# Performance work log

Hardware: AMD Instinct MI355X
Metric: run time of the kernel (lower is better)

Reference implementation:

```python
import jax, jax.numpy as jnp
import numpy as np

D_MODEL = 1024
N_HEADS = 16
HEAD_DIM = D_MODEL // N_HEADS


def setup_inputs() -> dict:
    key = jax.random.key(0)
    kx, kq, kk, kv, ko = jax.random.split(key, 5)
    B, T = 4, 2048
    s = 1.0 / np.sqrt(D_MODEL)
    return {
        "x": jax.random.normal(kx, (B, T, D_MODEL), dtype=jnp.float32),
        "W_Q": jax.random.normal(kq, (D_MODEL, D_MODEL), dtype=jnp.float32) * s,
        "W_K": jax.random.normal(kk, (D_MODEL, D_MODEL), dtype=jnp.float32) * s,
        "W_V": jax.random.normal(kv, (D_MODEL, D_MODEL), dtype=jnp.float32) * s,
        "W_O": jax.random.normal(ko, (D_MODEL, D_MODEL), dtype=jnp.float32) * s,
    }


def reference(x, W_Q, W_K, W_V, W_O):
    B, T, C = x.shape
    H, hd = N_HEADS, HEAD_DIM
    # nn.Linear applies x @ W.T; W_* here are the [out,in] weight matrices.
    def proj(W):
        return (x @ W.T).reshape(B, T, H, hd).transpose(0, 2, 1, 3)  # [B,H,T,hd]
    q, k, v = proj(W_Q), proj(W_K), proj(W_V)
    scale = 1.0 / np.sqrt(hd).astype(np.float32)
    attn = jnp.einsum("bhqd,bhkd->bhqk", q, k) * scale  # [B,H,T,T]
    causal = jnp.tril(jnp.ones((T, T), dtype=bool))
    attn = jnp.where(causal, attn, -jnp.inf)
    attn = jax.nn.softmax(attn, axis=-1)
    out = jnp.einsum("bhqk,bhkd->bhqd", attn, v)  # [B,H,T,hd]
    out = out.transpose(0, 2, 1, 3).reshape(B, T, C)
    return out @ W_O.T
```

## Files before the change

### kernel.cpp

```cpp
#include <hip/hip_runtime.h>
#include <hip/hip_bf16.h>
#include <stdint.h>


typedef __attribute__((ext_vector_type(8))) short short8;
typedef __attribute__((ext_vector_type(4))) short short4v;
typedef __attribute__((ext_vector_type(4))) float floatx4;

#define LOG2E 1.4426950408889634f

__device__ __forceinline__ void gload_lds16(const void* g, void* l) {
  __builtin_amdgcn_global_load_lds(
      (const __attribute__((address_space(1))) void*)g,
      (__attribute__((address_space(3))) void*)l, 16, 0, 0);
}

__device__ __forceinline__ short f2bf(float f) {
  __hip_bfloat16 h = __float2bfloat16(f);
  return *reinterpret_cast<short*>(&h);
}

__global__ __launch_bounds__(256) void cvt_f32_bf16(const float* __restrict__ src,
                                                    short* __restrict__ dst, int n4,
                                                    float scale) {
  const int i = blockIdx.x * blockDim.x + threadIdx.x;
  if (i >= n4) return;
  const float4 v = reinterpret_cast<const float4*>(src)[i];
  short4v o;
  o.x = f2bf(v.x * scale); o.y = f2bf(v.y * scale);
  o.z = f2bf(v.z * scale); o.w = f2bf(v.w * scale);
  reinterpret_cast<short4v*>(dst)[i] = o;
}

__global__ __launch_bounds__(256) void cvt_weights(const float* __restrict__ wq,
                                                   const float* __restrict__ wk,
                                                   const float* __restrict__ wv,
                                                   const float* __restrict__ wo,
                                                   short* __restrict__ dst0,
                                                   float qscale) {
  const int y = blockIdx.y;
  const float* src = (y == 0) ? wq : (y == 1) ? wk : (y == 2) ? wv : wo;
  const float scale = (y == 0) ? qscale : 1.0f;
  short* dst = dst0 + (size_t)y * 1048576;
  const int i = blockIdx.x * blockDim.x + threadIdx.x;
  const float4 v = reinterpret_cast<const float4*>(src)[i];
  short4v o;
  o.x = f2bf(v.x * scale); o.y = f2bf(v.y * scale);
  o.z = f2bf(v.z * scale); o.w = f2bf(v.w * scale);
  reinterpret_cast<short4v*>(&dst[i * 4])[0] = o;
}

__global__ __launch_bounds__(512) void gemm_qkv(
    const short* __restrict__ xb, const short* __restrict__ wqkv,
    short* __restrict__ Qb, short* __restrict__ Kb, short* __restrict__ Vt) {
  __shared__ short lds_a[3][256 * 32];
  __shared__ short lds_b[3][3 * 128 * 32];
  const int tid = threadIdx.x;
  const int lane = tid & 63;
  const int w = tid >> 6;
  const int wm = w >> 1, wn = w & 1;
  const int lrow = lane & 15, lgrp = lane >> 4;

  const int flat = blockIdx.x;
  const int n0 = (flat & 7) * 128;
  const int m0 = (flat >> 3) * 256;

  floatx4 acc[3][4][4] = {};

  const int srow = tid >> 2;
  const int scb = (tid & 3) ^ (srow & 3) ^ ((srow & 4) >> 1);
  const short* ag = xb + (size_t)(m0 + srow) * 1024 + scb * 8;
  const short* bg = wqkv + (size_t)(n0 + srow) * 1024 + scb * 8;

  auto stage5 = [&](short* la, short* lb) {
    gload_lds16(ag, la + tid * 8);
    gload_lds16(ag + 128 * 1024, la + (512 + tid) * 8);
    gload_lds16(bg,           lb + tid * 8);
    gload_lds16(bg + 1048576, lb + 4096 + tid * 8);
    gload_lds16(bg + 2097152, lb + 8192 + tid * 8);
    ag += 32; bg += 32;
  };

  const int slA = (lgrp ^ (lrow & 3) ^ ((lrow & 4) >> 1)) * 8;

  auto tile = [&](const short* la, const short* lb, short* na, short* nb, bool pf) {
    if (pf) stage5(na, nb);
    short8 af[4];
#pragma unroll
    for (int mf = 0; mf < 4; ++mf)
      af[mf] = *reinterpret_cast<const short8*>(
          &la[(wm * 64 + mf * 16 + lrow) * 32 + slA]);
#pragma unroll
    for (int z = 0; z < 3; ++z) {
      short8 bf[4];
#pragma unroll
      for (int nf = 0; nf < 4; ++nf)
        bf[nf] = *reinterpret_cast<const short8*>(
            &lb[z * 4096 + (wn * 64 + nf * 16 + lrow) * 32 + slA]);
      __builtin_amdgcn_s_setprio(1);
#pragma unroll
      for (int mf = 0; mf < 4; ++mf)
#pragma unroll
        for (int nf = 0; nf < 4; ++nf)
          acc[z][mf][nf] = __builtin_amdgcn_mfma_f32_16x16x32_bf16(
              af[mf], bf[nf], acc[z][mf][nf], 0, 0, 0);
      __builtin_amdgcn_s_setprio(0);
    }
  };

  auto tiletop = [&](int n) {
    __builtin_amdgcn_sched_barrier(0);
    if (n == 0)
      asm volatile("s_waitcnt vmcnt(0)" ::: "memory");
    else
      asm volatile("s_waitcnt vmcnt(5)" ::: "memory");
    __builtin_amdgcn_s_barrier();
    __builtin_amdgcn_sched_barrier(0);
  };

  stage5(lds_a[0], lds_b[0]);
  stage5(lds_a[1], lds_b[1]);

#pragma unroll 1
  for (int kt = 0; kt < 30; kt += 3) {
    tiletop(5); tile(lds_a[0], lds_b[0], lds_a[2], lds_b[2], true);
    tiletop(5); tile(lds_a[1], lds_b[1], lds_a[0], lds_b[0], true);
    tiletop(5); tile(lds_a[2], lds_b[2], lds_a[1], lds_b[1], true);
  }
  tiletop(5); tile(lds_a[0], lds_b[0], nullptr, nullptr, false);
  tiletop(0); tile(lds_a[1], lds_b[1], nullptr, nullptr, false);

#pragma unroll
  for (int z = 0; z < 3; ++z) {
#pragma unroll
    for (int mf = 0; mf < 4; ++mf) {
#pragma unroll
      for (int nf = 0; nf < 4; ++nf) {
        if (z == 2) {
          short4v pk;
#pragma unroll
          for (int r = 0; r < 4; ++r) pk[r] = f2bf(acc[z][mf][nf][r]);
          const int t0 = m0 + wm * 64 + mf * 16 + lgrp * 4;
          const int ch = n0 + wn * 64 + nf * 16 + lrow;
          const int bh = ((t0 >> 11) << 4) + (ch >> 6);
          *reinterpret_cast<short4v*>(
              &Vt[(size_t)bh * 131072 + (size_t)(ch & 63) * 2048 + (t0 & 2047)]) = pk;
        } else {
          short* C = (z == 0) ? Qb : Kb;
#pragma unroll
          for (int r = 0; r < 4; ++r) {
            const int grow = m0 + wm * 64 + mf * 16 + lgrp * 4 + r;
            const int gcol = n0 + wn * 64 + nf * 16 + lrow;
            C[(size_t)grow * 1024 + gcol] = f2bf(acc[z][mf][nf][r]);
          }
        }
      }
    }
  }
}

template <int MODE>
__device__ __forceinline__ void gemm256_body(const short* __restrict__ A,
                                             const short* __restrict__ B,
                                             void* __restrict__ Cout,
                                             int m0, int n0,
                                             short* __restrict__ la0,
                                             short* __restrict__ la1,
                                             short* __restrict__ la2,
                                             short* __restrict__ lb0,
                                             short* __restrict__ lb1,
                                             short* __restrict__ lb2) {
  const int tid = threadIdx.x;
  const int lane = tid & 63;
  const int w = tid >> 6;
  const int wm = w >> 1, wn = w & 1;
  const int lrow = lane & 15, lgrp = lane >> 4;

  floatx4 acc[4][4] = {};

  const int srow = tid >> 2;
  const int scb = (tid & 3) ^ (srow & 3) ^ ((srow & 4) >> 1);
  const short* ag = A + (size_t)(m0 + srow) * 1024 + scb * 8;
  const short* bg = B + (size_t)(n0 + srow) * 1024 + scb * 8;

  auto stage3 = [&](short* la, short* lb) {
    gload_lds16(ag, la + tid * 8);
    gload_lds16(ag + 128 * 1024, la + (512 + tid) * 8);
    gload_lds16(bg, lb + tid * 8);
    ag += 32; bg += 32;
  };

  const int slA = (lgrp ^ (lrow & 3) ^ ((lrow & 4) >> 1)) * 8;

  auto tile = [&](const short* la, const short* lb, short* na, short* nb, bool pf) {
    if (pf) stage3(na, nb);
    short8 af[4], bf[4];
#pragma unroll
    for (int mf = 0; mf < 4; ++mf) {
      const int row = wm * 64 + mf * 16 + lrow;
      af[mf] = *reinterpret_cast<const short8*>(&la[row * 32 + slA]);
    }
#pragma unroll
    for (int nf = 0; nf < 4; ++nf) {
      const int row = wn * 64 + nf * 16 + lrow;
      bf[nf] = *reinterpret_cast<const short8*>(&lb[row * 32 + slA]);
    }
    __builtin_amdgcn_s_setprio(1);
#pragma unroll
    for (int mf = 0; mf < 4; ++mf)
#pragma unroll
      for (int nf = 0; nf < 4; ++nf)
        acc[mf][nf] = __builtin_amdgcn_mfma_f32_16x16x32_bf16(af[mf], bf[nf], acc[mf][nf], 0, 0, 0);
    __builtin_amdgcn_s_setprio(0);
  };

  auto tiletop = [&](int n) {
    __builtin_amdgcn_sched_barrier(0);
    if (n == 0)
      asm volatile("s_waitcnt vmcnt(0)" ::: "memory");
    else
      asm volatile("s_waitcnt vmcnt(3)" ::: "memory");
    __builtin_amdgcn_s_barrier();
    __builtin_amdgcn_sched_barrier(0);
  };

  stage3(la0, lb0);
  stage3(la1, lb1);

#pragma unroll 1
  for (int kt = 0; kt < 30; kt += 3) {
    tiletop(3); tile(la0, lb0, la2, lb2, true);
    tiletop(3); tile(la1, lb1, la0, lb0, true);
    tiletop(3); tile(la2, lb2, la1, lb1, true);
  }
  tiletop(3); tile(la0, lb0, nullptr, nullptr, false);
  tiletop(0); tile(la1, lb1, nullptr, nullptr, false);

#pragma unroll
  for (int mf = 0; mf < 4; ++mf) {
#pragma unroll
    for (int nf = 0; nf < 4; ++nf) {
#pragma unroll
      for (int r = 0; r < 4; ++r) {
        const int grow = m0 + wm * 64 + mf * 16 + lgrp * 4 + r;
        const int gcol = n0 + wn * 64 + nf * 16 + lrow;
        if (MODE == 1)
          reinterpret_cast<short*>(Cout)[(size_t)grow * 1024 + gcol] = f2bf(acc[mf][nf][r]);
        else
          reinterpret_cast<float*>(Cout)[(size_t)grow * 1024 + gcol] = acc[mf][nf][r];
      }
    }
  }
}

__global__ __launch_bounds__(512) void gemm_out(const short* __restrict__ Ob,
                                                const short* __restrict__ wo,
                                                float* __restrict__ out) {
  __shared__ short lds_a[3][256 * 32];
  __shared__ short lds_b[3][128 * 32];
  const int flat = blockIdx.x;
  const int xcd = flat & 7, rest = flat >> 3;
  const int nblk = rest & 7, pg = rest >> 3;
  const int panel = pg * 8 + xcd;
  gemm256_body<0>(Ob, wo, out, panel * 256, nblk * 128,
                  lds_a[0], lds_a[1], lds_a[2], lds_b[0], lds_b[1], lds_b[2]);
}

__global__ __launch_bounds__(256, 4) void attn_fwd(const short* __restrict__ Q,
                                                   const short* __restrict__ K,
                                                   const short* __restrict__ Vt,
                                                   short* __restrict__ O) {
  __shared__ short lds_k[2][64 * 64];
  __shared__ short lds_v[2][64 * 64];
  __shared__ short lds_p[4][16 * 64];

  const int tid = threadIdx.x;
  const int lane = tid & 63;
  const int w = tid >> 6;
  const int lrow = lane & 15, lgrp = lane >> 4;
  const int flat = blockIdx.x;
  const int bh = flat & 63;
  const int p = flat >> 6;
  const int qc = 4 * (((p & 3) + (p >> 2)) & 3) + (p >> 2);
  const int b = bh >> 4, h = bh & 15;

  const size_t base = (size_t)b * 2048 * 1024 + h * 64;
  const size_t vbase = (size_t)bh * 131072;

  const int srow = tid >> 3;
  const int scb = (tid & 7) ^ (srow & 7);
  const size_t koff = (size_t)srow * 1024 + scb * 8;
  const size_t voff = (size_t)srow * 2048 + scb * 8;
  short* const kd0 = &lds_k[0][tid * 8];
  short* const kd1 = &lds_k[1][tid * 8];
  short* const vd0 = &lds_v[0][tid * 8];
  short* const vd1 = &lds_v[1][tid * 8];

  auto stageK = [&](short* ldst, const short* gsrc) {
    gload_lds16(gsrc, ldst);
    gload_lds16(gsrc + 32 * 1024, ldst + 2048);
  };
  auto stageV = [&](short* ldst, const short* gsrc) {
    gload_lds16(gsrc, ldst);
    gload_lds16(gsrc + 32 * 2048, ldst + 2048);
  };

  const int qw = qc * 128 + w * 32;
  const int lastkb = 2 * qc + (w >> 1);
  const int nkb = 2 * qc + 2;

  short8 qf[2][2];
#pragma unroll
  for (int qt = 0; qt < 2; ++qt) {
    const short* qp = Q + base + (size_t)(qw + qt * 16 + lrow) * 1024 + lgrp * 8;
    qf[qt][0] = *reinterpret_cast<const short8*>(qp);
    qf[qt][1] = *reinterpret_cast<const short8*>(qp + 32);
  }

  floatx4 oacc[2][4] = {};
  float lsum0 = 0.f, lsum1 = 0.f;

  const short* kg = K + base + koff;
  const short* vg = Vt + vbase + voff;

  auto body = [&](int kb, const short* __restrict__ ldsk,
                  const short* __restrict__ ldsv) {
    if (kb > lastkb) return;
    floatx4 s[2][4];
    __builtin_amdgcn_s_setprio(1);
#pragma unroll
    for (int nf = 0; nf < 4; ++nf) {
      const short8 kf0 = *reinterpret_cast<const short8*>(
          &ldsk[(nf * 16 + lrow) * 64 + ((lgrp) ^ (lrow & 7)) * 8]);
      const short8 kf1 = *reinterpret_cast<const short8*>(
          &ldsk[(nf * 16 + lrow) * 64 + ((4 + lgrp) ^ (lrow & 7)) * 8]);
#pragma unroll
      for (int qt = 0; qt < 2; ++qt) {
        floatx4 z = {};
        z = __builtin_amdgcn_mfma_f32_16x16x32_bf16(kf0, qf[qt][0], z, 0, 0, 0);
        z = __builtin_amdgcn_mfma_f32_16x16x32_bf16(kf1, qf[qt][1], z, 0, 0, 0);
        s[qt][nf] = z;
      }
    }
    __builtin_amdgcn_s_setprio(0);

    if (kb == lastkb) {
#pragma unroll
      for (int qt = 0; qt < 2; ++qt)
#pragma unroll
        for (int nf = 0; nf < 4; ++nf)
#pragma unroll
          for (int r = 0; r < 4; ++r) {
            const int kg_ = kb * 64 + nf * 16 + lgrp * 4 + r;
            const int qg_ = qw + qt * 16 + lrow;
            if (kg_ > qg_) s[qt][nf][r] = -1e30f;
          }
    }

    short8 pa[2][2];
    const int c8w = (lgrp) ;
#pragma unroll
    for (int qt = 0; qt < 2; ++qt) {
      float ls = 0.f;
#pragma unroll
      for (int nf = 0; nf < 4; ++nf) {
        const float p0 = __builtin_amdgcn_exp2f(s[qt][nf][0]);
        const float p1 = __builtin_amdgcn_exp2f(s[qt][nf][1]);
        const float p2 = __builtin_amdgcn_exp2f(s[qt][nf][2]);
        const float p3 = __builtin_amdgcn_exp2f(s[qt][nf][3]);
        ls += (p0 + p1) + (p2 + p3);
        short4v pk;
        pk.x = f2bf(p0); pk.y = f2bf(p1); pk.z = f2bf(p2); pk.w = f2bf(p3);
        const int c8 = (nf * 4 + lgrp) ^ ((lrow & 7) << 1);
        *reinterpret_cast<short4v*>(&lds_p[w][lrow * 64 + c8 * 4]) = pk;
      }
      if (qt == 0) lsum0 += ls; else lsum1 += ls;
      const int c0 = ((lgrp) ^ (lrow & 7)) * 8;
      const int c1 = ((4 + lgrp) ^ (lrow & 7)) * 8;
      pa[qt][0] = *reinterpret_cast<const short8*>(&lds_p[w][lrow * 64 + c0]);
      pa[qt][1] = *reinterpret_cast<const short8*>(&lds_p[w][lrow * 64 + c1]);
    }

    __builtin_amdgcn_s_setprio(1);
#pragma unroll
    for (int nf = 0; nf < 4; ++nf) {
      const short8 vf0 = *reinterpret_cast<const short8*>(
          &ldsv[(nf * 16 + lrow) * 64 + ((lgrp) ^ (lrow & 7)) * 8]);
      const short8 vf1 = *reinterpret_cast<const short8*>(
          &ldsv[(nf * 16 + lrow) * 64 + ((4 + lgrp) ^ (lrow & 7)) * 8]);
#pragma unroll
      for (int qt = 0; qt < 2; ++qt) {
        oacc[qt][nf] = __builtin_amdgcn_mfma_f32_16x16x32_bf16(pa[qt][0], vf0, oacc[qt][nf], 0, 0, 0);
        oacc[qt][nf] = __builtin_amdgcn_mfma_f32_16x16x32_bf16(pa[qt][1], vf1, oacc[qt][nf], 0, 0, 0);
      }
    }
    __builtin_amdgcn_s_setprio(0);
  };

  stageK(kd0, kg); kg += 65536;
  stageV(vd0, vg); vg += 64;
  __syncthreads();

#pragma unroll 1
  for (int kb = 0; kb < nkb; kb += 2) {
    if (kb + 1 < nkb) { stageK(kd1, kg); kg += 65536; stageV(vd1, vg); vg += 64; }
    body(kb, lds_k[0], lds_v[0]);
    __syncthreads();
    if (kb + 1 >= nkb) break;
    if (kb + 2 < nkb) { stageK(kd0, kg); kg += 65536; stageV(vd0, vg); vg += 64; }
    body(kb + 1, lds_k[1], lds_v[1]);
    __syncthreads();
  }

  lsum0 += __shfl_xor(lsum0, 16, 64);
  lsum0 += __shfl_xor(lsum0, 32, 64);
  lsum1 += __shfl_xor(lsum1, 16, 64);
  lsum1 += __shfl_xor(lsum1, 32, 64);
#pragma unroll
  for (int qt = 0; qt < 2; ++qt) {
    const float lw = qt == 0 ? lsum0 : lsum1;
#pragma unroll
    for (int r = 0; r < 4; ++r) {
      const float linv = 1.0f / __shfl(lw, lgrp * 4 + r, 64);
      const int t = qw + qt * 16 + lgrp * 4 + r;
#pragma unroll
      for (int nf = 0; nf < 4; ++nf)
        O[base + (size_t)t * 1024 + nf * 16 + lrow] = f2bf(oacc[qt][nf][r] * linv);
    }
  }
}

extern "C" void kernel_launch(void* const* d_in, const int* in_sizes, int n_in,
                              void* d_out, int out_size, void* d_ws, size_t ws_size,
                              hipStream_t stream) {
  const float* x  = (const float*)d_in[0];
  const float* Wq = (const float*)d_in[1];
  const float* Wk = (const float*)d_in[2];
  const float* Wv = (const float*)d_in[3];
  const float* Wo = (const float*)d_in[4];

  uint8_t* ws = (uint8_t*)d_ws;
  short* xb  = (short*)(ws + 0);
  short* wqb = (short*)(ws + 16777216);
  short* wob = (short*)(ws + 23068672);
  short* Qb  = (short*)(ws + 25165824);
  short* Kb  = (short*)(ws + 41943040);
  short* Vt  = (short*)(ws + 58720256);
  short* Ob  = (short*)(ws + 75497472);
  if (ws_size < 92274688ull) return;

  const float qscale = 0.125f * LOG2E;

  cvt_f32_bf16<<<8192, 256, 0, stream>>>(x, xb, 2097152, 1.0f);
  cvt_weights<<<dim3(1024, 4), 256, 0, stream>>>(Wq, Wk, Wv, Wo, wqb, qscale);

  gemm_qkv<<<256, 512, 0, stream>>>(xb, wqb, Qb, Kb, Vt);
  attn_fwd<<<1024, 256, 0, stream>>>(Qb, Kb, Vt, Ob);
  gemm_out<<<256, 512, 0, stream>>>(Ob, wob, (float*)d_out);
}
```

Measured before the change: 147.8 us.

## Restructure QKV GEMM into 256x256 tiles with BK=64 and XCD-aware mapping

Rewrites the fused QKV projection GEMM. Each block previously computed a 256x128 tile across Q, K and V together with K-step 32 and triple buffering. Now each block computes a single 256x256 output tile of the concatenated QKV weight, with K-step 64, double buffering, and prefetches split into quarter-tile phases with barriers between MFMA groups. The grid grows from 256 to 384 blocks, and block indices are remapped so each XCD handles contiguous M rows, aiming for better L2 reuse and more MFMA work per LDS read. The cost is more barriers per K-step and heavier LDS and register use, which may lower occupancy.

After: 163.9 us. 1.11x slower.

```diff
diff --git a/kernel.cpp b/kernel.cpp
--- a/kernel.cpp
+++ b/kernel.cpp
@@ -53,110 +53,186 @@
 __global__ __launch_bounds__(512) void gemm_qkv(
     const short* __restrict__ xb, const short* __restrict__ wqkv,
     short* __restrict__ Qb, short* __restrict__ Kb, short* __restrict__ Vt) {
-  __shared__ short lds_a[3][256 * 32];
-  __shared__ short lds_b[3][3 * 128 * 32];
+  __shared__ short lA[2][256 * 64];
+  __shared__ short lB[2][256 * 64];
   const int tid = threadIdx.x;
   const int lane = tid & 63;
   const int w = tid >> 6;
-  const int wm = w >> 1, wn = w & 1;
+  const int wm = w >> 2, wn = w & 3;
   const int lrow = lane & 15, lgrp = lane >> 4;
 
   const int flat = blockIdx.x;
-  const int n0 = (flat & 7) * 128;
-  const int m0 = (flat >> 3) * 256;
-
-  floatx4 acc[3][4][4] = {};
-
-  const int srow = tid >> 2;
-  const int scb = (tid & 3) ^ (srow & 3) ^ ((srow & 4) >> 1);
+  const int xcd = flat & 7, j = flat >> 3;
+  const int m0 = (xcd * 4 + j / 12) * 256;
+  const int n0 = (j % 12) * 256;
+
+  floatx4 acc[8][4] = {};
+
+  const int srow = tid >> 3;
+  const int scb = (tid & 7) ^ (srow & 7);
   const short* ag = xb + (size_t)(m0 + srow) * 1024 + scb * 8;
   const short* bg = wqkv + (size_t)(n0 + srow) * 1024 + scb * 8;
 
-  auto stage5 = [&](short* la, short* lb) {
-    gload_lds16(ag, la + tid * 8);
-    gload_lds16(ag + 128 * 1024, la + (512 + tid) * 8);
-    gload_lds16(bg,           lb + tid * 8);
-    gload_lds16(bg + 1048576, lb + 4096 + tid * 8);
-    gload_lds16(bg + 2097152, lb + 8192 + tid * 8);
-    ag += 32; bg += 32;
-  };
-
-  const int slA = (lgrp ^ (lrow & 3) ^ ((lrow & 4) >> 1)) * 8;
-
-  auto tile = [&](const short* la, const short* lb, short* na, short* nb, bool pf) {
-    if (pf) stage5(na, nb);
-    short8 af[4];
-#pragma unroll
-    for (int mf = 0; mf < 4; ++mf)
-      af[mf] = *reinterpret_cast<const short8*>(
-          &la[(wm * 64 + mf * 16 + lrow) * 32 + slA]);
-#pragma unroll
-    for (int z = 0; z < 3; ++z) {
-      short8 bf[4];
-#pragma unroll
-      for (int nf = 0; nf < 4; ++nf)
-        bf[nf] = *reinterpret_cast<const short8*>(
-            &lb[z * 4096 + (wn * 64 + nf * 16 + lrow) * 32 + slA]);
-      __builtin_amdgcn_s_setprio(1);
+  auto stA = [&](int buf, int h, int kt) {
+    const short* s = ag + (size_t)kt * 64 + (size_t)h * 131072;
+    gload_lds16(s, &lA[buf][(h * 1024 + tid) * 8]);
+    gload_lds16(s + 65536, &lA[buf][(h * 1024 + 512 + tid) * 8]);
+  };
+  auto stB = [&](int buf, int h, int kt) {
+    const short* s = bg + (size_t)kt * 64 + (size_t)h * 131072;
+    gload_lds16(s, &lB[buf][(h * 1024 + tid) * 8]);
+    gload_lds16(s + 65536, &lB[buf][(h * 1024 + 512 + tid) * 8]);
+  };
+
+  auto rdA = [&](int buf, int mf, int ks) {
+    const int row = wm * 128 + mf * 16 + lrow;
+    return *reinterpret_cast<const short8*>(
+        &lA[buf][row * 64 + (((ks * 4 + lgrp) ^ (lrow & 7)) * 8)]);
+  };
+  auto rdB = [&](int buf, int nf, int ks) {
+    const int row = wn * 64 + nf * 16 + lrow;
+    return *reinterpret_cast<const short8*>(
+        &lB[buf][row * 64 + (((ks * 4 + lgrp) ^ (lrow & 7)) * 8)]);
+  };
+
+#define MIDBAR_LGKM                                            \
+  __builtin_amdgcn_sched_barrier(0);                           \
+  __builtin_amdgcn_s_barrier();                                \
+  asm volatile("s_waitcnt lgkmcnt(0)" ::: "memory");           \
+  __builtin_amdgcn_sched_barrier(0);
+#define MIDBAR_PLAIN                                           \
+  __builtin_amdgcn_sched_barrier(0);                           \
+  __builtin_amdgcn_s_barrier();                                \
+  __builtin_amdgcn_sched_barrier(0);
+#define ENDBAR                                                 \
+  __builtin_amdgcn_sched_barrier(0);                           \
+  __builtin_amdgcn_s_barrier();                                \
+  __builtin_amdgcn_sched_barrier(0);
+
+  auto tile4 = [&](int cbuf, int kt, bool pfAo, bool pfBs, int vmend) {
+    const int obuf = cbuf ^ 1;
+    short8 aL[2][4], aH[2][4], b[2][4];
+#pragma unroll
+    for (int ks = 0; ks < 2; ++ks) {
+#pragma unroll
+      for (int mf = 0; mf < 4; ++mf) aL[ks][mf] = rdA(cbuf, mf, ks);
+      b[ks][0] = rdB(cbuf, 0, ks);
+      b[ks][1] = rdB(cbuf, 1, ks);
+    }
+    if (pfAo) stA(obuf, 0, kt + 1);
+    MIDBAR_LGKM;
+    __builtin_amdgcn_s_setprio(1);
+#pragma unroll
+    for (int ks = 0; ks < 2; ++ks)
 #pragma unroll
       for (int mf = 0; mf < 4; ++mf)
 #pragma unroll
-        for (int nf = 0; nf < 4; ++nf)
-          acc[z][mf][nf] = __builtin_amdgcn_mfma_f32_16x16x32_bf16(
-              af[mf], bf[nf], acc[z][mf][nf], 0, 0, 0);
-      __builtin_amdgcn_s_setprio(0);
-    }
-  };
-
-  auto tiletop = [&](int n) {
+        for (int nf = 0; nf < 2; ++nf)
+          acc[mf][nf] = __builtin_amdgcn_mfma_f32_16x16x32_bf16(aL[ks][mf], b[ks][nf], acc[mf][nf], 0, 0, 0);
+    __builtin_amdgcn_s_setprio(0);
+    ENDBAR;
+#pragma unroll
+    for (int ks = 0; ks < 2; ++ks) {
+      b[ks][2] = rdB(cbuf, 2, ks);
+      b[ks][3] = rdB(cbuf, 3, ks);
+    }
+    if (pfAo) stA(obuf, 1, kt + 1);
+    MIDBAR_LGKM;
+    __builtin_amdgcn_s_setprio(1);
+#pragma unroll
+    for (int ks = 0; ks < 2; ++ks)
+#pragma unroll
+      for (int mf = 0; mf < 4; ++mf)
+#pragma unroll
+        for (int nf = 2; nf < 4; ++nf)
+          acc[mf][nf] = __builtin_amdgcn_mfma_f32_16x16x32_bf16(aL[ks][mf], b[ks][nf], acc[mf][nf], 0, 0, 0);
+    __builtin_amdgcn_s_setprio(0);
+    ENDBAR;
+#pragma unroll
+    for (int ks = 0; ks < 2; ++ks)
+#pragma unroll
+      for (int mf = 0; mf < 4; ++mf) aH[ks][mf] = rdA(cbuf, 4 + mf, ks);
+    if (pfBs) stB(cbuf, 0, kt + 2);
+    MIDBAR_LGKM;
+    __builtin_amdgcn_s_setprio(1);
+#pragma unroll
+    for (int ks = 0; ks < 2; ++ks)
+#pragma unroll
+      for (int mf = 0; mf < 4; ++mf)
+#pragma unroll
+        for (int nf = 0; nf < 2; ++nf)
+          acc[4 + mf][nf] = __builtin_amdgcn_mfma_f32_16x16x32_bf16(aH[ks][mf], b[ks][nf], acc[4 + mf][nf], 0, 0, 0);
+    __builtin_amdgcn_s_setprio(0);
+    ENDBAR;
+    if (pfBs) stB(cbuf, 1, kt + 2);
+    MIDBAR_PLAIN;
+    __builtin_amdgcn_s_setprio(1);
+#pragma unroll
+    for (int ks = 0; ks < 2; ++ks)
+#pragma unroll
+      for (int mf = 0; mf < 4; ++mf)
+#pragma unroll
+        for (int nf = 2; nf < 4; ++nf)
+          acc[4 + mf][nf] = __builtin_amdgcn_mfma_f32_16x16x32_bf16(aH[ks][mf], b[ks][nf], acc[4 + mf][nf], 0, 0, 0);
+    __builtin_amdgcn_s_setprio(0);
     __builtin_amdgcn_sched_barrier(0);
-    if (n == 0)
-      asm volatile("s_waitcnt vmcnt(0)" ::: "memory");
-    else
-      asm volatile("s_waitcnt vmcnt(5)" ::: "memory");
+    if (vmend == 4) asm volatile("s_waitcnt vmcnt(4)" ::: "memory");
+    else if (vmend == 0) asm volatile("s_waitcnt vmcnt(0)" ::: "memory");
     __builtin_amdgcn_s_barrier();
     __builtin_amdgcn_sched_barrier(0);
   };
 
-  stage5(lds_a[0], lds_b[0]);
-  stage5(lds_a[1], lds_b[1]);
+  stA(0, 0, 0); stA(0, 1, 0);
+  stB(0, 0, 0); stB(0, 1, 0);
+  stB(1, 0, 1); stB(1, 1, 1);
+  asm volatile("s_waitcnt vmcnt(4)" ::: "memory");
+  __builtin_amdgcn_s_barrier();
+  __builtin_amdgcn_sched_barrier(0);
 
 #pragma unroll 1
-  for (int kt = 0; kt < 30; kt += 3) {
-    tiletop(5); tile(lds_a[0], lds_b[0], lds_a[2], lds_b[2], true);
-    tiletop(5); tile(lds_a[1], lds_b[1], lds_a[0], lds_b[0], true);
-    tiletop(5); tile(lds_a[2], lds_b[2], lds_a[1], lds_b[1], true);
-  }
-  tiletop(5); tile(lds_a[0], lds_b[0], nullptr, nullptr, false);
-  tiletop(0); tile(lds_a[1], lds_b[1], nullptr, nullptr, false);
-
-#pragma unroll
-  for (int z = 0; z < 3; ++z) {
-#pragma unroll
-    for (int mf = 0; mf < 4; ++mf) {
+  for (int i = 0; i < 7; ++i) {
+    const int t = 2 * i;
+    tile4(0, t, true, true, 4);
+    tile4(1, t + 1, true, true, 4);
+  }
+  tile4(0, 14, true, false, 0);
+  tile4(1, 15, false, false, -1);
+
+  const int z = n0 >> 10;
+  const int colbase = (n0 & 1023) + wn * 64;
+  if (z == 2) {
+#pragma unroll
+    for (int mf = 0; mf < 8; ++mf) {
 #pragma unroll
       for (int nf = 0; nf < 4; ++nf) {
-        if (z == 2) {
-          short4v pk;
-#pragma unroll
-          for (int r = 0; r < 4; ++r) pk[r] = f2bf(acc[z][mf][nf][r]);
-          const int t0 = m0 + wm * 64 + mf * 16 + lgrp * 4;
-          const int ch = n0 + wn * 64 + nf * 16 + lrow;
-          const int bh = ((t0 >> 11) << 4) + (ch >> 6);
-          *reinterpret_cast<short4v*>(
-              &Vt[(size_t)bh * 131072 + (size_t)(ch & 63) * 2048 + (t0 & 2047)]) = pk;
-        } else {
-          short* C = (z == 0) ? Qb : Kb;
-#pragma unroll
-          for (int r = 0; r < 4; ++r) {
-            const int grow = m0 + wm * 64 + mf * 16 + lgrp * 4 + r;
-            const int gcol = n0 + wn * 64 + nf * 16 + lrow;
-            C[(size_t)grow * 1024 + gcol] = f2bf(acc[z][mf][nf][r]);
-          }
+        short4v pk;
+#pragma unroll
+        for (int r = 0; r < 4; ++r) pk[r] = f2bf(acc[mf][nf][r]);
+        const int t0 = m0 + wm * 128 + mf * 16 + lgrp * 4;
+        const int ch = colbase + nf * 16 + lrow;
+        const int bh = ((t0 >> 11) << 4) + (ch >> 6);
+        *reinterpret_cast<short4v*>(
+            &Vt[(size_t)bh * 131072 + (size_t)(ch & 63) * 2048 + (t0 & 2047)]) = pk;
+      }
+    }
+  } else {
+    short* C = (z == 0) ? Qb : Kb;
+#pragma unroll
+    for (int mf = 0; mf < 8; ++mf) {
+#pragma unroll
+      for (int nf = 0; nf < 4; ++nf) {
+#pragma unroll
+        for (int r = 0; r < 4; ++r) {
+          const int grow = m0 + wm * 128 + mf * 16 + lgrp * 4 + r;
+          const int gcol = colbase + nf * 16 + lrow;
+          C[(size_t)grow * 1024 + gcol] = f2bf(acc[mf][nf][r]);
         }
       }
     }
   }
+#undef MIDBAR_LGKM
+#undef MIDBAR_PLAIN
+#undef ENDBAR
 }
 
 template <int MODE>
@@ -358,7 +434,6 @@
     }
 
     short8 pa[2][2];
-    const int c8w = (lgrp) ;
 #pragma unroll
     for (int qt = 0; qt < 2; ++qt) {
       float ls = 0.f;
@@ -454,7 +529,7 @@
   cvt_f32_bf16<<<8192, 256, 0, stream>>>(x, xb, 2097152, 1.0f);
   cvt_weights<<<dim3(1024, 4), 256, 0, stream>>>(Wq, Wk, Wv, Wo, wqb, qscale);
 
-  gemm_qkv<<<256, 512, 0, stream>>>(xb, wqb, Qb, Kb, Vt);
+  gemm_qkv<<<384, 512, 0, stream>>>(xb, wqb, Qb, Kb, Vt);
   attn_fwd<<<1024, 256, 0, stream>>>(Qb, Kb, Vt, Ob);
   gemm_out<<<256, 512, 0, stream>>>(Ob, wob, (float*)d_out);
 }
```
